# Performance work log

Measured on AMD Instinct MI355X. Metric: run time of the kernel, lower is better.

## Reference

```python
import jax, jax.numpy as jnp
import numpy as np

B, S, D = 2, 2048, 2048
H, KV, HD = 8, 2, 256
EPS = 1e-6
WINDOW = 512
ROPE_THETA = 1000000.0
NEG = -1e9


def setup_inputs() -> dict:
    key = jax.random.key(0)
    ks = jax.random.split(key, 6)
    hidden_states = jax.random.normal(ks[0], (B, S, D), dtype=jnp.float32)
    # rotary tables: [S, HD//2] freqs tiled to [B, S, HD]
    inv_freq = 1.0 / (ROPE_THETA ** (np.arange(0, HD, 2, dtype=np.float32) / HD))
    pos = np.arange(S, dtype=np.float32)
    freqs = np.outer(pos, inv_freq)                      # [S, HD/2]
    emb = np.concatenate([freqs, freqs], axis=-1)        # [S, HD]
    cos = jnp.broadcast_to(jnp.asarray(np.cos(emb))[None], (B, S, HD))
    sin = jnp.broadcast_to(jnp.asarray(np.sin(emb))[None], (B, S, HD))
    # causal sliding-window additive mask: allow k<=q and q-k < WINDOW
    q_idx = np.arange(S)[:, None]
    k_idx = np.arange(S)[None, :]
    allowed = (k_idx <= q_idx) & (q_idx - k_idx < WINDOW)
    attention_mask = jnp.asarray(np.where(allowed, 0.0, NEG).astype(np.float32))[None, None]
    sc = 0.02
    wq = jax.random.normal(ks[1], (D, H * HD), dtype=jnp.float32) * sc
    wk = jax.random.normal(ks[2], (D, KV * HD), dtype=jnp.float32) * sc
    wv = jax.random.normal(ks[3], (D, KV * HD), dtype=jnp.float32) * sc
    wo = jax.random.normal(ks[4], (H * HD, D), dtype=jnp.float32) * sc
    q_norm_w = jnp.ones((HD,), dtype=jnp.float32)
    k_norm_w = jnp.ones((HD,), dtype=jnp.float32)
    return dict(hidden_states=hidden_states, cos=cos, sin=sin,
                attention_mask=attention_mask, wq=wq, wk=wk, wv=wv, wo=wo,
                q_norm_w=q_norm_w, k_norm_w=k_norm_w)


def _rms_norm(x, w):
    xf = x.astype(jnp.float32)
    y = xf * jax.lax.rsqrt(jnp.mean(xf * xf, axis=-1, keepdims=True) + EPS)
    return (y * w).astype(x.dtype)


def _apply_rope(x, cos, sin):
    # x: [B, S, N, HD]; cos/sin: [B, S, HD] -> unsqueeze at dim 2
    c = cos[:, :, None, :]
    s = sin[:, :, None, :]
    x1, x2 = jnp.split(x, 2, axis=-1)
    rot = jnp.concatenate([-x2, x1], axis=-1)
    return x * c + rot * s


def reference(hidden_states, cos, sin, attention_mask, wq, wk, wv, wo,
              q_norm_w, k_norm_w):
    b, s, _ = hidden_states.shape
    n_rep = H // KV
    q = (hidden_states @ wq).reshape(b, s, H, HD)
    q = _apply_rope(_rms_norm(q, q_norm_w), cos, sin).transpose(0, 2, 1, 3)   # [B,H,S,HD]
    k = (hidden_states @ wk).reshape(b, s, KV, HD)
    k = _apply_rope(_rms_norm(k, k_norm_w), cos, sin).transpose(0, 2, 1, 3)   # [B,KV,S,HD]
    v = (hidden_states @ wv).reshape(b, s, KV, HD)
    v = _rms_norm(v, jnp.float32(1.0)).transpose(0, 2, 1, 3)                  # [B,KV,S,HD]
    k = jnp.repeat(k, n_rep, axis=1)  # GQA repeat_kv -> [B,H,S,HD]
    v = jnp.repeat(v, n_rep, axis=1)
    # Gemma3n uses scaling = 1.0 (QK-RMSNorm replaces 1/sqrt(d))
    scores = jnp.einsum('bhqd,bhkd->bhqk', q, k) + attention_mask[:, :, :, :s]
    probs = jax.nn.softmax(scores.astype(jnp.float32), axis=-1).astype(q.dtype)
    out = jnp.einsum('bhqk,bhkd->bhqd', probs, v)
    out = out.transpose(0, 2, 1, 3).reshape(b, s, H * HD)
    return out @ wo
```

## Files before the change

kernel.cpp:

```cpp
#include <hip/hip_runtime.h>
#include <hip/hip_bf16.h>
#include <hip/hip_fp16.h>

#define B_ 2
#define S_ 2048
#define D_ 2048
#define H_ 8
#define KV_ 2
#define HD_ 256
#define WINDOW_ 512
#define EPS_ 1e-6f
#define MASKV_ -30000.0f

typedef _Float16 f16;
typedef _Float16 half8 __attribute__((ext_vector_type(8)));
typedef _Float16 half2v __attribute__((ext_vector_type(2)));
typedef _Float16 half4v __attribute__((ext_vector_type(4)));
typedef float floatx4 __attribute__((ext_vector_type(4)));
typedef float floatx8 __attribute__((ext_vector_type(8)));
typedef float floatx16 __attribute__((ext_vector_type(16)));

#define GLOAD_LDS16(g, l)                                                        \
    __builtin_amdgcn_global_load_lds(                                            \
        (const __attribute__((address_space(1))) unsigned int*)(g),              \
        (__attribute__((address_space(3))) unsigned int*)(l), 16, 0, 0)

__global__ __launch_bounds__(256) void prep(const float* __restrict__ x,
                                            const float* __restrict__ wq,
                                            const float* __restrict__ wk,
                                            const float* __restrict__ wv,
                                            const float* __restrict__ wo,
                                            f16* __restrict__ xh,
                                            f16* __restrict__ BT,
                                            f16* __restrict__ woT) {
    int bid = blockIdx.x;
    const int t = threadIdx.x;
    if (bid < 8192) {
        const int i = bid * 256 + t;
        float4 v = ((const float4*)x)[i];
        half4v hv = {(f16)v.x, (f16)v.y, (f16)v.z, (f16)v.w};
        ((half4v*)xh)[i] = hv;
        return;
    }
    bid -= 8192;
    const float* src;
    f16* dst;
    int C, bx, by;
    if (bid < 1024) {
        src = wq; dst = BT; C = 2048; bx = bid & 31; by = bid >> 5;
    } else if (bid < 1280) {
        const int b3 = bid - 1024;
        src = wk; dst = BT + (size_t)2048 * 2048; C = 512; bx = b3 & 7; by = b3 >> 3;
    } else if (bid < 1536) {
        const int b3 = bid - 1280;
        src = wv; dst = BT + (size_t)2560 * 2048; C = 512; bx = b3 & 7; by = b3 >> 3;
    } else {
        const int b3 = bid - 1536;
        src = wo; dst = woT; C = 2048; bx = b3 & 31; by = b3 >> 5;
    }
    __shared__ float tl[64][65];
    const int c0 = bx * 64, r0 = by * 64;
#pragma unroll
    for (int i = 0; i < 4; ++i) {
        const int idx = i * 256 + t;
        const int row = idx >> 4;
        const int c4 = (idx & 15) * 4;
        float4 v = *(const float4*)&src[(size_t)(r0 + row) * C + c0 + c4];
        tl[row][c4 + 0] = v.x; tl[row][c4 + 1] = v.y;
        tl[row][c4 + 2] = v.z; tl[row][c4 + 3] = v.w;
    }
    __syncthreads();
#pragma unroll
    for (int i = 0; i < 4; ++i) {
        const int idx = i * 256 + t;
        const int c = idx >> 4;
        const int r4 = (idx & 15) * 4;
        half4v hv = {(f16)tl[r4 + 0][c], (f16)tl[r4 + 1][c],
                     (f16)tl[r4 + 2][c], (f16)tl[r4 + 3][c]};
        *(half4v*)&dst[(size_t)(c0 + c) * 2048 + r0 + r4] = hv;
    }
}

#define CH_ 528
template <typename OutT>
__global__ __launch_bounds__(256) void gemm_f16(const f16* __restrict__ A,
                                                const f16* __restrict__ BT,
                                                OutT* __restrict__ C,
                                                int M, int N, int K) {
    __shared__ __align__(16) f16 sA[16 * CH_];
    __shared__ __align__(16) f16 sB[16 * CH_];

    const int t = threadIdx.x;
    const int lane = t & 63;
    const int w = t >> 6;
    const int l31 = lane & 31, q1 = lane >> 5;
    const int m0 = blockIdx.y * 128, n0 = blockIdx.x * 128;
    const int mw = (w & 1) * 64, nw = (w >> 1) * 64;

    floatx16 acc[4];
#pragma unroll
    for (int i = 0; i < 4; ++i) acc[i] = (floatx16)(0.f);

    const int r8 = lane >> 3;
    const int g = (lane & 7) ^ r8;

    for (int k0 = 0; k0 < K; k0 += 64) {
#pragma unroll
        for (int cc = 0; cc < 4; ++cc) {
            const int chunk = w * 4 + cc;
            const int row = chunk * 8 + r8;
            GLOAD_LDS16(A + (size_t)(m0 + row) * K + k0 + g * 8,
                        sA + chunk * CH_ + lane * 8);
            GLOAD_LDS16(BT + (size_t)(n0 + row) * K + k0 + g * 8,
                        sB + chunk * CH_ + lane * 8);
        }
        __syncthreads();

#pragma unroll
        for (int ks = 0; ks < 4; ++ks) {
            const int G = ks * 2 + q1;
            half8 af[2], bf[2];
#pragma unroll
            for (int mt = 0; mt < 2; ++mt) {
                const int ra = mw + mt * 32 + l31;
                af[mt] = *(const half8*)(sA + (ra >> 3) * CH_ + (ra & 7) * 64 +
                                         (G ^ (ra & 7)) * 8);
                const int rb = nw + mt * 32 + l31;
                bf[mt] = *(const half8*)(sB + (rb >> 3) * CH_ + (rb & 7) * 64 +
                                         (G ^ (rb & 7)) * 8);
            }
#pragma unroll
            for (int mt = 0; mt < 2; ++mt)
#pragma unroll
                for (int nt = 0; nt < 2; ++nt)
                    acc[mt * 2 + nt] = __builtin_amdgcn_mfma_f32_32x32x16_f16(
                        af[mt], bf[nt], acc[mt * 2 + nt], 0, 0, 0);
        }
        __syncthreads();
    }

#pragma unroll
    for (int mt = 0; mt < 2; ++mt)
#pragma unroll
        for (int nt = 0; nt < 2; ++nt)
#pragma unroll
            for (int r = 0; r < 16; ++r) {
                const int row = m0 + mw + mt * 32 + (r & 3) + 8 * (r >> 2) + 4 * q1;
                const int col = n0 + nw + nt * 32 + l31;
                C[(size_t)row * N + col] = (OutT)acc[mt * 2 + nt][r];
            }
}

#define NRBK_ ((B_ * S_ * KV_) / 4)

__global__ __launch_bounds__(256) void norm_kv_f16(
    const f16* __restrict__ QKVh, f16* __restrict__ Kh, f16* __restrict__ Vt,
    const float* __restrict__ cosb, const float* __restrict__ sinb,
    const float* __restrict__ kw) {
    __shared__ f16 vt[64][266];

    const int w = threadIdx.x >> 6, lane = threadIdx.x & 63;

    if (blockIdx.x < NRBK_) {
        const int wid = blockIdx.x * 4 + w;
        const int d0 = lane * 2;
        const int b = wid / (S_ * KV_);
        const int r = wid % (S_ * KV_);
        const int s = r / KV_, kv = r % KV_;
        const f16* p = QKVh + (size_t)(b * S_ + s) * 3072 + 2048 + kv * HD_;
        half2v lo = *(const half2v*)(p + d0);
        half2v hi = *(const half2v*)(p + 128 + d0);
        float x0 = (float)lo[0], x1 = (float)lo[1], x2 = (float)hi[0], x3 = (float)hi[1];
        float ss = x0 * x0 + x1 * x1 + x2 * x2 + x3 * x3;
#pragma unroll
        for (int off = 32; off >= 1; off >>= 1) ss += __shfl_xor(ss, off);
        const float inv = rsqrtf(ss * (1.0f / HD_) + EPS_);
        float2 wlo = *(const float2*)(kw + d0), whi = *(const float2*)(kw + 128 + d0);
        float y0 = x0 * inv * wlo.x, y1 = x1 * inv * wlo.y;
        float y2 = x2 * inv * whi.x, y3 = x3 * inv * whi.y;
        const float* cb = cosb + (size_t)(b * S_ + s) * HD_;
        const float* sb = sinb + (size_t)(b * S_ + s) * HD_;
        float2 clo = *(const float2*)(cb + d0), chi = *(const float2*)(cb + 128 + d0);
        float2 slo = *(const float2*)(sb + d0), shi = *(const float2*)(sb + 128 + d0);
        half2v olo = {(f16)(y0 * clo.x - y2 * slo.x), (f16)(y1 * clo.y - y3 * slo.y)};
        half2v ohi = {(f16)(y2 * chi.x + y0 * shi.x), (f16)(y3 * chi.y + y1 * shi.y)};
        f16* d = Kh + ((size_t)(b * KV_ + kv) * S_ + s) * HD_;
        *(half2v*)(d + d0) = olo;
        *(half2v*)(d + 128 + d0) = ohi;
        return;
    }

    const int vb = blockIdx.x - NRBK_;
    const int s0 = (vb & 31) * 64;
    const int kv = (vb >> 5) & 1;
    const int b  = vb >> 6;

    for (int r = 0; r < 16; ++r) {
        const int sl = w * 16 + r;
        const f16* p = QKVh + (size_t)(b * S_ + s0 + sl) * 3072 + 2560 + kv * HD_;
        const int d0 = lane * 2;
        half2v lo = *(const half2v*)(p + d0);
        half2v hi = *(const half2v*)(p + 128 + d0);
        float x0 = (float)lo[0], x1 = (float)lo[1], x2 = (float)hi[0], x3 = (float)hi[1];
        float ss = x0 * x0 + x1 * x1 + x2 * x2 + x3 * x3;
#pragma unroll
        for (int off = 32; off >= 1; off >>= 1) ss += __shfl_xor(ss, off);
        const float inv = rsqrtf(ss * (1.0f / HD_) + EPS_);
        half2v olo = {(f16)(x0 * inv), (f16)(x1 * inv)};
        half2v ohi = {(f16)(x2 * inv), (f16)(x3 * inv)};
        *(half2v*)&vt[sl][d0] = olo;
        *(half2v*)&vt[sl][128 + d0] = ohi;
    }
    __syncthreads();
    f16* dst = Vt + (size_t)(b * KV_ + kv) * HD_ * S_;
    for (int i = 0; i < 64; ++i) {
        const int dd = w * 64 + i;
        dst[(size_t)dd * S_ + s0 + lane] = vt[lane][dd];
    }
}

__global__ __launch_bounds__(512, 2) void attn_mfma(const f16* __restrict__ QKVh,
                                                    const f16* __restrict__ Kh,
                                                    const f16* __restrict__ Vt,
                                                    f16* __restrict__ attnh,
                                                    const float* __restrict__ cosb,
                                                    const float* __restrict__ sinb,
                                                    const float* __restrict__ qw) {
    __shared__ __align__(16) f16 sK[2][64 * 256];
    __shared__ __align__(16) f16 sV[2][256 * 64];
    __shared__ __align__(16) f16 sP[8][16 * 72];

    const int qt = blockIdx.x, h = blockIdx.y, b = blockIdx.z;
    const int kvh = h / (H_ / KV_);
    const int t = threadIdx.x, lane = t & 63, w = t >> 6;
    const int i16 = lane & 15, q4 = lane >> 4;

    const int qrow = qt * 128 + w * 16 + i16;
    const f16* qbase = QKVh + (size_t)(b * S_ + qrow) * 3072 + h * HD_ + q4 * 8;
    half8 qf[8];
#pragma unroll
    for (int kk = 0; kk < 8; ++kk) qf[kk] = *(const half8*)(qbase + kk * 32);

    {
        float ss = 0.f;
#pragma unroll
        for (int kk = 0; kk < 8; ++kk)
#pragma unroll
            for (int j = 0; j < 8; ++j) {
                const float v = (float)qf[kk][j];
                ss += v * v;
            }
        ss += __shfl_xor(ss, 16);
        ss += __shfl_xor(ss, 32);
        const float inv = rsqrtf(ss * (1.0f / HD_) + EPS_);
        const float* cb = cosb + (size_t)(b * S_ + qrow) * HD_ + q4 * 8;
        const float* sb = sinb + (size_t)(b * S_ + qrow) * HD_ + q4 * 8;
        const float* wp = qw + q4 * 8;
#pragma unroll
        for (int kk = 0; kk < 4; ++kk) {
            const int dl = kk * 32, dh = dl + 128;
            floatx8 cl = *(const floatx8*)(cb + dl);
            floatx8 ch = *(const floatx8*)(cb + dh);
            floatx8 sl = *(const floatx8*)(sb + dl);
            floatx8 sh = *(const floatx8*)(sb + dh);
            floatx8 wl = *(const floatx8*)(wp + dl);
            floatx8 wh = *(const floatx8*)(wp + dh);
            half8 nl, nh;
#pragma unroll
            for (int j = 0; j < 8; ++j) {
                const float xl = (float)qf[kk][j] * inv * wl[j];
                const float xh = (float)qf[kk + 4][j] * inv * wh[j];
                nl[j] = (f16)(xl * cl[j] - xh * sl[j]);
                nh[j] = (f16)(xh * ch[j] + xl * sh[j]);
            }
            qf[kk] = nl;
            qf[kk + 4] = nh;
        }
    }

    floatx4 o[16];
#pragma unroll
    for (int i = 0; i < 16; ++i) o[i] = (floatx4){0.f, 0.f, 0.f, 0.f};
    float mrow[4] = {-1e30f, -1e30f, -1e30f, -1e30f};
    float lrow[4] = {0.f, 0.f, 0.f, 0.f};

    const size_t kbase = (size_t)(b * KV_ + kvh) * S_ * HD_;
    const size_t vbase = (size_t)(b * KV_ + kvh) * HD_ * S_;
    const int srow0 = qt * 128 + w * 16 + q4 * 4;

    const int kt_lo = (2 * qt - 8) > 0 ? (2 * qt - 8) : 0;
    const int kt_hi = 2 * qt + 1;
    const int s_lo_w = qt * 128 + w * 16;
    int ktw_lo = (s_lo_w - (WINDOW_ - 1)) >> 6;
    if (ktw_lo < kt_lo) ktw_lo = kt_lo;
    const int ktw_hi = (s_lo_w + 15) >> 6;

    auto stage = [&](int kt, int buf) {
#pragma unroll
        for (int c = 0; c < 4; ++c) {
            const int chunk = w * 4 + c;
            const int keyl = chunk * 2 + (lane >> 5);
            const int g = (lane & 31) ^ (keyl & 31);
            GLOAD_LDS16(Kh + kbase + (size_t)(kt * 64 + keyl) * HD_ + g * 8,
                        sK[buf] + chunk * 512 + lane * 8);
            const int diml = chunk * 8 + (lane >> 3);
            const int g2 = (lane & 7) ^ (diml & 7);
            GLOAD_LDS16(Vt + vbase + (size_t)diml * S_ + kt * 64 + g2 * 8,
                        sV[buf] + chunk * 512 + lane * 8);
        }
    };

    stage(kt_lo, 0);
    int cur = 0;
    for (int kt = kt_lo; kt <= kt_hi; ++kt, cur ^= 1) {
        __syncthreads();
        if (kt < kt_hi) stage(kt + 1, cur ^ 1);
        if (kt < ktw_lo || kt > ktw_hi) continue;

        const f16* sKc = sK[cur];
        const f16* sVc = sV[cur];

        floatx4 sc[4];
#pragma unroll
        for (int nt = 0; nt < 4; ++nt) sc[nt] = (floatx4){0.f, 0.f, 0.f, 0.f};
#pragma unroll
        for (int ks = 0; ks < 8; ++ks)
#pragma unroll
            for (int nt = 0; nt < 4; ++nt) {
                const int keyl = nt * 16 + i16;
                const int gp = (ks * 4 + q4) ^ (keyl & 31);
                half8 kf = *(const half8*)(sKc + keyl * 256 + gp * 8);
                sc[nt] = __builtin_amdgcn_mfma_f32_16x16x32_f16(qf[ks], kf, sc[nt], 0, 0, 0);
            }

#pragma unroll
        for (int r = 0; r < 4; ++r) {
            const int s = srow0 + r;
            float mx = -1e30f;
#pragma unroll
            for (int nt = 0; nt < 4; ++nt) {
                const int j = kt * 64 + nt * 16 + i16;
                const bool valid = (j <= s) && (s - j < WINDOW_);
                const float v = valid ? sc[nt][r] : MASKV_;
                sc[nt][r] = v;
                mx = fmaxf(mx, v);
            }
#pragma unroll
            for (int off = 1; off < 16; off <<= 1) mx = fmaxf(mx, __shfl_xor(mx, off));
            const float mnew = fmaxf(mrow[r], mx);
            const float alpha = __expf(mrow[r] - mnew);
            mrow[r] = mnew;
            float rs = 0.f;
#pragma unroll
            for (int nt = 0; nt < 4; ++nt) {
                const float p = __expf(sc[nt][r] - mnew);
                sc[nt][r] = p;
                rs += p;
            }
#pragma unroll
            for (int off = 1; off < 16; off <<= 1) rs += __shfl_xor(rs, off);
            lrow[r] = lrow[r] * alpha + rs;
#pragma unroll
            for (int nt2 = 0; nt2 < 16; ++nt2) o[nt2][r] *= alpha;
        }

        f16* sPw = sP[w];
#pragma unroll
        for (int nt = 0; nt < 4; ++nt)
#pragma unroll
            for (int r = 0; r < 4; ++r)
                sPw[(q4 * 4 + r) * 72 + nt * 16 + i16] = (f16)sc[nt][r];
        asm volatile("s_waitcnt lgkmcnt(0)" ::: "memory");

#pragma unroll
        for (int kt2 = 0; kt2 < 2; ++kt2) {
            half8 pf = *(const half8*)(sPw + i16 * 72 + kt2 * 32 + q4 * 8);
#pragma unroll
            for (int nt2 = 0; nt2 < 16; ++nt2) {
                const int dim = nt2 * 16 + i16;
                const int gp = (kt2 * 4 + q4) ^ (dim & 7);
                half8 vf = *(const half8*)(sVc + dim * 64 + gp * 8);
                o[nt2] = __builtin_amdgcn_mfma_f32_16x16x32_f16(pf, vf, o[nt2], 0, 0, 0);
            }
        }
    }

    float inv2[4];
#pragma unroll
    for (int r = 0; r < 4; ++r) inv2[r] = 1.0f / lrow[r];
    f16* ob = attnh + (size_t)(b * S_ + qt * 128 + w * 16) * (H_ * HD_) + h * HD_;
#pragma unroll
    for (int nt2 = 0; nt2 < 16; ++nt2)
#pragma unroll
        for (int r = 0; r < 4; ++r)
            ob[(size_t)(q4 * 4 + r) * (H_ * HD_) + nt2 * 16 + i16] =
                (f16)(o[nt2][r] * inv2[r]);
}

extern "C" void kernel_launch(void* const* d_in, const int* in_sizes, int n_in,
                              void* d_out, int out_size, void* d_ws, size_t ws_size,
                              hipStream_t stream) {
    const float* x    = (const float*)d_in[0];
    const float* cosb = (const float*)d_in[1];
    const float* sinb = (const float*)d_in[2];
    const float* wq = (const float*)d_in[4];
    const float* wk = (const float*)d_in[5];
    const float* wv = (const float*)d_in[6];
    const float* wo = (const float*)d_in[7];
    const float* qw = (const float*)d_in[8];
    const float* kw = (const float*)d_in[9];
    float* out = (float*)d_out;

    f16* ws = (f16*)d_ws;
    f16* xh    = ws;
    f16* BT    = xh + 8388608;
    f16* woT   = BT + 6291456;
    f16* QKVh  = woT + 4194304;
    f16* Kh    = QKVh + 12582912;
    f16* Vt    = Kh + 2097152;
    f16* attnh = xh;

    const int M = B_ * S_;

    prep<<<8192 + 2560, 256, 0, stream>>>(x, wq, wk, wv, wo, xh, BT, woT);

    gemm_f16<f16><<<dim3(24, 32), 256, 0, stream>>>(xh, BT, QKVh, M, 3072, D_);

    norm_kv_f16<<<NRBK_ + 128, 256, 0, stream>>>(QKVh, Kh, Vt, cosb, sinb, kw);

    attn_mfma<<<dim3(S_ / 128, H_, B_), 512, 0, stream>>>(QKVh, Kh, Vt, attnh,
                                                          cosb, sinb, qw);

    gemm_f16<float><<<dim3(16, 32), 256, 0, stream>>>(attnh, woT, out, M, D_, H_ * HD_);
}
```

Baseline: 311.8 us.

## Replace GEMM with triple-buffered async-LDS ring and larger 256-row tiles

Replaces the single-buffered 128x128 GEMM with a templated kernel that keeps a three-slot LDS ring, issuing global-to-LDS loads two k-tiles ahead and waiting on vmcnt counts so copies overlap MFMA work. Tiles grow to 256xBN with a BK of 32, each wave now accumulates 128x64, and s_setprio is raised around the MFMA block. The goal is to hide memory latency and improve data reuse in the QKV and output projections. The cost is higher register and LDS use, and the hand-written vmcnt counts and barriers must stay correct for each template instance.

New measurement: 389.1 us. 24.8% more time.

```diff
diff --git a/kernel.cpp b/kernel.cpp
--- a/kernel.cpp
+++ b/kernel.cpp
@@ -81,73 +81,131 @@
     }
 }
 
-#define CH_ 528
-template <typename OutT>
-__global__ __launch_bounds__(256) void gemm_f16(const f16* __restrict__ A,
-                                                const f16* __restrict__ BT,
-                                                OutT* __restrict__ C,
-                                                int M, int N, int K) {
-    __shared__ __align__(16) f16 sA[16 * CH_];
-    __shared__ __align__(16) f16 sB[16 * CH_];
-
-    const int t = threadIdx.x;
-    const int lane = t & 63;
-    const int w = t >> 6;
+template <int BN, int NW, typename OutT>
+__global__ __launch_bounds__(NW * 64, 2) void gemm_ring(const f16* __restrict__ A,
+                                                        const f16* __restrict__ BT,
+                                                        OutT* __restrict__ C,
+                                                        int M, int N, int K) {
+    constexpr int ASZ = 8192;
+    constexpr int BSZ = BN * 32;
+    constexpr int LA = 16 / NW;
+    constexpr int LB = (BN / 16) / NW;
+    constexpr int VM = LA + LB;
+
+    __shared__ __align__(16) f16 sA[3 * ASZ];
+    __shared__ __align__(16) f16 sB[3 * BSZ];
+
+    const int tid = threadIdx.x;
+    const int lane = tid & 63, w = tid >> 6;
     const int l31 = lane & 31, q1 = lane >> 5;
-    const int m0 = blockIdx.y * 128, n0 = blockIdx.x * 128;
-    const int mw = (w & 1) * 64, nw = (w >> 1) * 64;
-
-    floatx16 acc[4];
-#pragma unroll
-    for (int i = 0; i < 4; ++i) acc[i] = (floatx16)(0.f);
-
-    const int r8 = lane >> 3;
-    const int g = (lane & 7) ^ r8;
-
-    for (int k0 = 0; k0 < K; k0 += 64) {
-#pragma unroll
-        for (int cc = 0; cc < 4; ++cc) {
-            const int chunk = w * 4 + cc;
-            const int row = chunk * 8 + r8;
-            GLOAD_LDS16(A + (size_t)(m0 + row) * K + k0 + g * 8,
-                        sA + chunk * CH_ + lane * 8);
-            GLOAD_LDS16(BT + (size_t)(n0 + row) * K + k0 + g * 8,
-                        sB + chunk * CH_ + lane * 8);
-        }
-        __syncthreads();
-
-#pragma unroll
-        for (int ks = 0; ks < 4; ++ks) {
-            const int G = ks * 2 + q1;
-            half8 af[2], bf[2];
-#pragma unroll
-            for (int mt = 0; mt < 2; ++mt) {
-                const int ra = mw + mt * 32 + l31;
-                af[mt] = *(const half8*)(sA + (ra >> 3) * CH_ + (ra & 7) * 64 +
-                                         (G ^ (ra & 7)) * 8);
-                const int rb = nw + mt * 32 + l31;
-                bf[mt] = *(const half8*)(sB + (rb >> 3) * CH_ + (rb & 7) * 64 +
-                                         (G ^ (rb & 7)) * 8);
-            }
-#pragma unroll
-            for (int mt = 0; mt < 2; ++mt)
-#pragma unroll
-                for (int nt = 0; nt < 2; ++nt)
-                    acc[mt * 2 + nt] = __builtin_amdgcn_mfma_f32_32x32x16_f16(
-                        af[mt], bf[nt], acc[mt * 2 + nt], 0, 0, 0);
-        }
-        __syncthreads();
-    }
-
-#pragma unroll
-    for (int mt = 0; mt < 2; ++mt)
-#pragma unroll
-        for (int nt = 0; nt < 2; ++nt)
+    const int m0 = blockIdx.y * 256, n0 = blockIdx.x * BN;
+    const int mw = (w & 1) * 128;
+    const int nw = (w >> 1) * 64;
+
+    const int sg = (lane >> 3) & 3;
+    const int sr7 = (lane & 7) ^ sg;
+    const int halfc = lane >> 5;
+
+    const f16* srcA[LA];
+    f16* dstA[LA];
+#pragma unroll
+    for (int i = 0; i < LA; ++i) {
+        const int pair = w * LA + i;
+        const int row = (pair * 2 + halfc) * 8 + sr7;
+        srcA[i] = A + (size_t)(m0 + row) * K + sg * 8;
+        dstA[i] = sA + pair * 512 + lane * 8;
+    }
+    const f16* srcB[LB];
+    f16* dstB[LB];
+#pragma unroll
+    for (int i = 0; i < LB; ++i) {
+        const int pair = w * LB + i;
+        const int row = (pair * 2 + halfc) * 8 + sr7;
+        srcB[i] = BT + (size_t)(n0 + row) * K + sg * 8;
+        dstB[i] = sB + pair * 512 + lane * 8;
+    }
+
+    auto stage = [&](int tile, int buf) {
+        const int ko = tile * 32;
+#pragma unroll
+        for (int i = 0; i < LA; ++i)
+            GLOAD_LDS16(srcA[i] + ko, dstA[i] + buf * ASZ);
+#pragma unroll
+        for (int i = 0; i < LB; ++i)
+            GLOAD_LDS16(srcB[i] + ko, dstB[i] + buf * BSZ);
+    };
+
+    const int arow = (l31 >> 3) * 256;
+    const int G0 = q1;
+    const int G1 = q1 + 2;
+    const int X0 = G0 * 8 + ((l31 & 7) ^ G0);
+    const int X1 = G1 * 8 + ((l31 & 7) ^ G1);
+    const int aoff0 = (mw >> 3) * 256 + arow + X0 * 8;
+    const int aoff1 = (mw >> 3) * 256 + arow + X1 * 8;
+    const int boff0 = (nw >> 3) * 256 + arow + X0 * 8;
+    const int boff1 = (nw >> 3) * 256 + arow + X1 * 8;
+
+    floatx16 acc[8];
+#pragma unroll
+    for (int i = 0; i < 8; ++i) acc[i] = (floatx16)(0.f);
+
+    const int NT = K >> 5;
+    stage(0, 0);
+    stage(1, 1);
+
+    int bsel = 0;
+    for (int t = 0; t < NT; ++t) {
+        if (t == NT - 1) {
+            asm volatile("s_waitcnt vmcnt(0)\n\ts_barrier" ::: "memory");
+        } else {
+            if constexpr (VM == 4)
+                asm volatile("s_waitcnt vmcnt(4)\n\ts_barrier" ::: "memory");
+            else
+                asm volatile("s_waitcnt vmcnt(6)\n\ts_barrier" ::: "memory");
+        }
+        const int b2 = bsel >= 1 ? bsel - 1 : 2;
+        if (t + 2 < NT) stage(t + 2, b2);
+
+        const f16* Ab = sA + bsel * ASZ;
+        const f16* Bb = sB + bsel * BSZ;
+        half8 a0[4], a1[4], b0[2], b1[2];
+#pragma unroll
+        for (int m = 0; m < 4; ++m) {
+            a0[m] = *(const half8*)(Ab + aoff0 + m * 1024);
+            a1[m] = *(const half8*)(Ab + aoff1 + m * 1024);
+        }
+#pragma unroll
+        for (int n = 0; n < 2; ++n) {
+            b0[n] = *(const half8*)(Bb + boff0 + n * 1024);
+            b1[n] = *(const half8*)(Bb + boff1 + n * 1024);
+        }
+        __builtin_amdgcn_s_setprio(1);
+#pragma unroll
+        for (int m = 0; m < 4; ++m)
+#pragma unroll
+            for (int n = 0; n < 2; ++n)
+                acc[m * 2 + n] = __builtin_amdgcn_mfma_f32_32x32x16_f16(
+                    a0[m], b0[n], acc[m * 2 + n], 0, 0, 0);
+#pragma unroll
+        for (int m = 0; m < 4; ++m)
+#pragma unroll
+            for (int n = 0; n < 2; ++n)
+                acc[m * 2 + n] = __builtin_amdgcn_mfma_f32_32x32x16_f16(
+                    a1[m], b1[n], acc[m * 2 + n], 0, 0, 0);
+        __builtin_amdgcn_s_setprio(0);
+
+        bsel = bsel == 2 ? 0 : bsel + 1;
+    }
+
+#pragma unroll
+    for (int m = 0; m < 4; ++m)
+#pragma unroll
+        for (int n = 0; n < 2; ++n)
 #pragma unroll
             for (int r = 0; r < 16; ++r) {
-                const int row = m0 + mw + mt * 32 + (r & 3) + 8 * (r >> 2) + 4 * q1;
-                const int col = n0 + nw + nt * 32 + l31;
-                C[(size_t)row * N + col] = (OutT)acc[mt * 2 + nt][r];
+                const int row = m0 + mw + m * 32 + (r & 3) + 8 * (r >> 2) + 4 * q1;
+                const int col = n0 + nw + n * 32 + l31;
+                C[(size_t)row * N + col] = (OutT)acc[m * 2 + n][r];
             }
 }
 
@@ -424,12 +482,13 @@
 
     prep<<<8192 + 2560, 256, 0, stream>>>(x, wq, wk, wv, wo, xh, BT, woT);
 
-    gemm_f16<f16><<<dim3(24, 32), 256, 0, stream>>>(xh, BT, QKVh, M, 3072, D_);
+    gemm_ring<256, 8, f16><<<dim3(12, 16), 512, 0, stream>>>(xh, BT, QKVh, M, 3072, D_);
 
     norm_kv_f16<<<NRBK_ + 128, 256, 0, stream>>>(QKVh, Kh, Vt, cosb, sinb, kw);
 
     attn_mfma<<<dim3(S_ / 128, H_, B_), 512, 0, stream>>>(QKVh, Kh, Vt, attnh,
                                                           cosb, sinb, qw);
 
-    gemm_f16<float><<<dim3(16, 32), 256, 0, stream>>>(attnh, woT, out, M, D_, H_ * HD_);
+    gemm_ring<128, 4, float><<<dim3(16, 16), 256, 0, stream>>>(attnh, woT, out,
+                                                               M, D_, H_ * HD_);
 }
```

## Replace QKV projection GEMM with 256x256 ping-pong pipelined 8-wave kernel

Applied to the files above, without the earlier changes.

Adds a new f16 GEMM kernel that uses 256x256 block tiles, 512 threads and four LDS quadrant slots. It issues direct global-to-LDS loads for the next K tile while MFMA 16x16x32 work runs on the current quadrant, uses XOR-swizzled LDS addressing, and raises wave priority around the MFMA sections. The kernel is used only for the QKV projection, with the aim of hiding memory latency and raising arithmetic intensity. The cost is a large LDS footprint and high register pressure, and the grid drops to 192 blocks, which may underfill the GPU.

Measured after the change: 313.7 us. No clear change (+0.6%).

```diff
diff --git a/kernel.cpp b/kernel.cpp
--- a/kernel.cpp
+++ b/kernel.cpp
@@ -1,6 +1,7 @@
 #include <hip/hip_runtime.h>
 #include <hip/hip_bf16.h>
 #include <hip/hip_fp16.h>
+#include <type_traits>
 
 #define B_ 2
 #define S_ 2048
@@ -24,6 +25,9 @@
     __builtin_amdgcn_global_load_lds(                                            \
         (const __attribute__((address_space(1))) unsigned int*)(g),              \
         (__attribute__((address_space(3))) unsigned int*)(l), 16, 0, 0)
+
+#define VMWAIT(n) asm volatile("s_waitcnt vmcnt(" #n ")" ::: "memory")
+#define IC(n) std::integral_constant<int, n>{}
 
 __global__ __launch_bounds__(256) void prep(const float* __restrict__ x,
                                             const float* __restrict__ wq,
@@ -151,6 +155,123 @@
             }
 }
 
+template <typename OutT>
+__global__ __launch_bounds__(512, 2) void gemm_8p(const f16* __restrict__ A,
+                                                  const f16* __restrict__ BT,
+                                                  OutT* __restrict__ C,
+                                                  int M, int N, int K) {
+    __shared__ __align__(16) f16 sAA[4 * 8192];
+    __shared__ __align__(16) f16 sBB[4 * 8192];
+
+    const int tid = threadIdx.x;
+    const int lane = tid & 63, w = tid >> 6;
+    const int i16 = lane & 15, q4 = lane >> 4;
+    const int w1 = w & 1, w2 = w >> 1;
+    const int m0 = blockIdx.y * 256, n0 = blockIdx.x * 256;
+
+    const int srow0 = tid >> 3;
+    const int kx = ((tid & 7) ^ ((tid >> 3) & 7)) * 8;
+    const f16* srcA0 = A + (size_t)(m0 + srow0) * K;
+    const f16* srcB0 = BT + (size_t)(n0 + srow0) * K;
+    f16* dstA0 = sAA + tid * 8;
+    f16* dstB0 = sBB + tid * 8;
+
+    auto stage = [&](int P, int kt) {
+        const int half = P >> 1;
+        const int slot = (2 * kt + half) & 3;
+        const int kb = kt * 64 + kx;
+        if ((P & 1) == 0) {
+            const f16* s = srcA0 + (size_t)(half * 128) * K + kb;
+            f16* d = dstA0 + slot * 8192;
+            GLOAD_LDS16(s, d);
+            GLOAD_LDS16(s + (size_t)64 * K, d + 4096);
+        } else {
+            const f16* s = srcB0 + (size_t)(half * 128) * K + kb;
+            f16* d = dstB0 + slot * 8192;
+            GLOAD_LDS16(s, d);
+            GLOAD_LDS16(s + (size_t)64 * K, d + 4096);
+        }
+    };
+
+    const int arow = (w1 * 64 + i16) * 64;
+    const int brow = (w2 * 32 + i16) * 64;
+    int xk[2];
+    xk[0] = ((0 + q4) ^ (i16 & 7)) * 8;
+    xk[1] = ((4 + q4) ^ (i16 & 7)) * 8;
+
+    floatx4 acc[4][4][2];
+#pragma unroll
+    for (int p = 0; p < 4; ++p)
+#pragma unroll
+        for (int mt = 0; mt < 4; ++mt)
+#pragma unroll
+            for (int nt = 0; nt < 2; ++nt)
+                acc[p][mt][nt] = (floatx4){0.f, 0.f, 0.f, 0.f};
+
+    int st = 0;
+
+    auto phase = [&](auto Pc, bool dostage, int ktn) {
+        constexpr int P = decltype(Pc)::value;
+        constexpr int qm = P & 1, qn = P >> 1;
+        __builtin_amdgcn_s_barrier();
+        const f16* ab = sAA + (size_t)(st + qm) * 8192;
+        const f16* bb = sBB + (size_t)(st + qn) * 8192;
+        half8 af[4][2], bf[2][2];
+#pragma unroll
+        for (int mt = 0; mt < 4; ++mt)
+#pragma unroll
+            for (int ks = 0; ks < 2; ++ks)
+                af[mt][ks] = *(const half8*)(ab + arow + mt * 1024 + xk[ks]);
+#pragma unroll
+        for (int nt = 0; nt < 2; ++nt)
+#pragma unroll
+            for (int ks = 0; ks < 2; ++ks)
+                bf[nt][ks] = *(const half8*)(bb + brow + nt * 1024 + xk[ks]);
+        if (dostage) stage(P, ktn);
+        __builtin_amdgcn_s_setprio(1);
+#pragma unroll
+        for (int mt = 0; mt < 4; ++mt)
+#pragma unroll
+            for (int nt = 0; nt < 2; ++nt)
+#pragma unroll
+                for (int ks = 0; ks < 2; ++ks)
+                    acc[P][mt][nt] = __builtin_amdgcn_mfma_f32_16x16x32_f16(
+                        af[mt][ks], bf[nt][ks], acc[P][mt][nt], 0, 0, 0);
+        __builtin_amdgcn_s_setprio(0);
+    };
+
+    const int NT = K >> 6;
+
+    stage(0, 0); stage(1, 0); stage(2, 0); stage(3, 0);
+
+    for (int T = 0; T < NT - 1; ++T) {
+        VMWAIT(4); phase(IC(0), true, T + 1);
+        VMWAIT(4); phase(IC(1), true, T + 1);
+        VMWAIT(4); phase(IC(2), true, T + 1);
+        phase(IC(3), true, T + 1);
+        st ^= 2;
+    }
+    VMWAIT(4); phase(IC(0), false, 0);
+    VMWAIT(2); phase(IC(1), false, 0);
+    VMWAIT(0); phase(IC(2), false, 0);
+    phase(IC(3), false, 0);
+
+#pragma unroll
+    for (int p = 0; p < 4; ++p) {
+        const int rb = m0 + (p & 1) * 128 + w1 * 64 + q4 * 4;
+        const int cb = n0 + (p >> 1) * 128 + w2 * 32 + i16;
+#pragma unroll
+        for (int mt = 0; mt < 4; ++mt)
+#pragma unroll
+            for (int nt = 0; nt < 2; ++nt) {
+                floatx4 v = acc[p][mt][nt];
+#pragma unroll
+                for (int r = 0; r < 4; ++r)
+                    C[(size_t)(rb + mt * 16 + r) * N + cb + nt * 16] = (OutT)v[r];
+            }
+    }
+}
+
 #define NRBK_ ((B_ * S_ * KV_) / 4)
 
 __global__ __launch_bounds__(256) void norm_kv_f16(
@@ -424,7 +545,7 @@
 
     prep<<<8192 + 2560, 256, 0, stream>>>(x, wq, wk, wv, wo, xh, BT, woT);
 
-    gemm_f16<f16><<<dim3(24, 32), 256, 0, stream>>>(xh, BT, QKVh, M, 3072, D_);
+    gemm_8p<f16><<<dim3(12, 16), 512, 0, stream>>>(xh, BT, QKVh, M, 3072, D_);
 
     norm_kv_f16<<<NRBK_ + 128, 256, 0, stream>>>(QKVh, Kh, Vt, cosb, sinb, kw);
 
```

## Add 256x256 eight-wave pipelined GEMM for QKV projection

Applied to the files above, without the earlier changes.

Adds a new 512-thread GEMM kernel with 256x256 tiles. It uses a four-slot LDS ring filled by direct global-to-LDS loads, explicit vmcnt waits, raw barriers and s_setprio, so loads for the next K-tile overlap with MFMA work on quadrants of the current tile. The QKV projection now uses this kernel in place of the old 128x128-tile GEMM. The larger tile improves data reuse, but the grid shrinks to 192 blocks, which may underfill the GPU's compute units. The hand-tuned wait counts also add correctness risk.

New measurement: 314.6 us. About the same (+0.9%).

```diff
diff --git a/kernel.cpp b/kernel.cpp
--- a/kernel.cpp
+++ b/kernel.cpp
@@ -1,6 +1,7 @@
 #include <hip/hip_runtime.h>
 #include <hip/hip_bf16.h>
 #include <hip/hip_fp16.h>
+#include <type_traits>
 
 #define B_ 2
 #define S_ 2048
@@ -24,6 +25,8 @@
     __builtin_amdgcn_global_load_lds(                                            \
         (const __attribute__((address_space(1))) unsigned int*)(g),              \
         (__attribute__((address_space(3))) unsigned int*)(l), 16, 0, 0)
+
+#define VMWAIT(n) asm volatile("s_waitcnt vmcnt(" #n ")" ::: "memory")
 
 __global__ __launch_bounds__(256) void prep(const float* __restrict__ x,
                                             const float* __restrict__ wq,
@@ -151,6 +154,156 @@
             }
 }
 
+template <typename OutT>
+__global__ __launch_bounds__(512, 2) void gemm_8p(const f16* __restrict__ A,
+                                                  const f16* __restrict__ BT,
+                                                  OutT* __restrict__ C,
+                                                  int M, int N, int K) {
+    __shared__ __align__(16) f16 sAA[4 * 8192];
+    __shared__ __align__(16) f16 sBB[4 * 8192];
+
+    const int tid = threadIdx.x;
+    const int lane = tid & 63, w = tid >> 6;
+    const int l31 = lane & 31, q1 = lane >> 5;
+    const int w1 = w & 1, w2 = w >> 1;
+    const int m0 = blockIdx.y * 256, n0 = blockIdx.x * 256;
+
+    const int kx = ((tid & 7) ^ ((tid >> 3) & 7)) * 8;
+    const f16* srcA0 = A + (size_t)(m0 + (tid >> 3)) * K;
+    const f16* srcB0 = BT + (size_t)(n0 + (tid >> 3)) * K;
+    f16* dstA0 = sAA + tid * 8;
+    f16* dstB0 = sBB + tid * 8;
+
+    auto stageA = [&](int half, int kt) {
+        const int slot = (2 * kt + half) & 3;
+        const f16* s = srcA0 + (size_t)(half * 128) * K + kt * 64 + kx;
+        f16* d = dstA0 + slot * 8192;
+        GLOAD_LDS16(s, d);
+        GLOAD_LDS16(s + (size_t)64 * K, d + 4096);
+    };
+    auto stageB = [&](int half, int kt) {
+        const int slot = (2 * kt + half) & 3;
+        const f16* s = srcB0 + (size_t)(half * 128) * K + kt * 64 + kx;
+        f16* d = dstB0 + slot * 8192;
+        GLOAD_LDS16(s, d);
+        GLOAD_LDS16(s + (size_t)64 * K, d + 4096);
+    };
+
+    const int arow = (w1 * 64 + l31) * 64;
+    const int brow = (w2 * 32 + l31) * 64;
+    int xk[4];
+#pragma unroll
+    for (int ks = 0; ks < 4; ++ks) xk[ks] = ((ks * 2 + q1) ^ (l31 & 7)) * 8;
+
+    floatx16 acc[4][2];
+#pragma unroll
+    for (int p = 0; p < 4; ++p)
+#pragma unroll
+        for (int mt = 0; mt < 2; ++mt) acc[p][mt] = (floatx16)(0.f);
+
+    int st = 0;
+
+    const int NT = K >> 6;
+
+    stageA(0, 0); stageB(0, 0); stageB(1, 0); stageA(1, 0);
+
+    auto tile = [&](auto LASTC, int T) {
+        constexpr bool LAST = decltype(LASTC)::value;
+        const f16* a0p = sAA + (size_t)(st + 0) * 8192;
+        const f16* a1p = sAA + (size_t)(st + 1) * 8192;
+        const f16* b0p = sBB + (size_t)(st + 0) * 8192;
+        const f16* b1p = sBB + (size_t)(st + 1) * 8192;
+        half8 a0[2][4], a1[2][4], bf[4];
+
+        VMWAIT(4);
+        __builtin_amdgcn_s_barrier();
+#pragma unroll
+        for (int mt = 0; mt < 2; ++mt)
+#pragma unroll
+            for (int ks = 0; ks < 4; ++ks)
+                a0[mt][ks] = *(const half8*)(a0p + arow + mt * 2048 + xk[ks]);
+#pragma unroll
+        for (int ks = 0; ks < 4; ++ks)
+            bf[ks] = *(const half8*)(b0p + brow + xk[ks]);
+        if constexpr (!LAST) stageA(0, T + 1);
+        __builtin_amdgcn_s_setprio(1);
+#pragma unroll
+        for (int ks = 0; ks < 4; ++ks)
+#pragma unroll
+            for (int mt = 0; mt < 2; ++mt)
+                acc[0][mt] = __builtin_amdgcn_mfma_f32_32x32x16_f16(
+                    a0[mt][ks], bf[ks], acc[0][mt], 0, 0, 0);
+        __builtin_amdgcn_s_setprio(0);
+
+        if constexpr (!LAST) VMWAIT(4); else VMWAIT(2);
+        __builtin_amdgcn_s_barrier();
+#pragma unroll
+        for (int ks = 0; ks < 4; ++ks)
+            bf[ks] = *(const half8*)(b1p + brow + xk[ks]);
+        if constexpr (!LAST) stageB(0, T + 1);
+        __builtin_amdgcn_s_setprio(1);
+#pragma unroll
+        for (int ks = 0; ks < 4; ++ks)
+#pragma unroll
+            for (int mt = 0; mt < 2; ++mt)
+                acc[1][mt] = __builtin_amdgcn_mfma_f32_32x32x16_f16(
+                    a0[mt][ks], bf[ks], acc[1][mt], 0, 0, 0);
+        __builtin_amdgcn_s_setprio(0);
+
+        if constexpr (!LAST) VMWAIT(4); else VMWAIT(0);
+        __builtin_amdgcn_s_barrier();
+#pragma unroll
+        for (int mt = 0; mt < 2; ++mt)
+#pragma unroll
+            for (int ks = 0; ks < 4; ++ks)
+                a1[mt][ks] = *(const half8*)(a1p + arow + mt * 2048 + xk[ks]);
+        if constexpr (!LAST) stageB(1, T + 1);
+        __builtin_amdgcn_s_setprio(1);
+#pragma unroll
+        for (int ks = 0; ks < 4; ++ks)
+#pragma unroll
+            for (int mt = 0; mt < 2; ++mt)
+                acc[2][mt] = __builtin_amdgcn_mfma_f32_32x32x16_f16(
+                    a1[mt][ks], bf[ks], acc[2][mt], 0, 0, 0);
+        __builtin_amdgcn_s_setprio(0);
+
+        __builtin_amdgcn_s_barrier();
+#pragma unroll
+        for (int ks = 0; ks < 4; ++ks)
+            bf[ks] = *(const half8*)(b0p + brow + xk[ks]);
+        if constexpr (!LAST) stageA(1, T + 1);
+        __builtin_amdgcn_s_setprio(1);
+#pragma unroll
+        for (int ks = 0; ks < 4; ++ks)
+#pragma unroll
+            for (int mt = 0; mt < 2; ++mt)
+                acc[3][mt] = __builtin_amdgcn_mfma_f32_32x32x16_f16(
+                    a1[mt][ks], bf[ks], acc[3][mt], 0, 0, 0);
+        __builtin_amdgcn_s_setprio(0);
+    };
+
+    for (int T = 0; T < NT - 1; ++T) {
+        tile(std::false_type{}, T);
+        st ^= 2;
+    }
+    tile(std::true_type{}, NT - 1);
+
+    const int qmv[4] = {0, 0, 1, 1};
+    const int qnv[4] = {0, 1, 1, 0};
+#pragma unroll
+    for (int p = 0; p < 4; ++p) {
+        const int rb = m0 + qmv[p] * 128 + w1 * 64;
+        const int cb = n0 + qnv[p] * 128 + w2 * 32 + l31;
+#pragma unroll
+        for (int mt = 0; mt < 2; ++mt)
+#pragma unroll
+            for (int r = 0; r < 16; ++r) {
+                const int row = rb + mt * 32 + (r & 3) + 8 * (r >> 2) + 4 * q1;
+                C[(size_t)row * N + cb] = (OutT)acc[p][mt][r];
+            }
+    }
+}
+
 #define NRBK_ ((B_ * S_ * KV_) / 4)
 
 __global__ __launch_bounds__(256) void norm_kv_f16(
@@ -424,7 +577,7 @@
 
     prep<<<8192 + 2560, 256, 0, stream>>>(x, wq, wk, wv, wo, xh, BT, woT);
 
-    gemm_f16<f16><<<dim3(24, 32), 256, 0, stream>>>(xh, BT, QKVh, M, 3072, D_);
+    gemm_8p<f16><<<dim3(12, 16), 512, 0, stream>>>(xh, BT, QKVh, M, 3072, D_);
 
     norm_kv_f16<<<NRBK_ + 128, 256, 0, stream>>>(QKVh, Kh, Vt, cosb, sinb, kw);
 
```
